# Optimization experiments

Hardware: AMD Instinct MI355X
Metric: run time of the kernel (lower is better)

## Reference

```python
import jax, jax.numpy as jnp
import numpy as np

BINS = [16]*20 + [32]*10 + [64]*5 + [65]  # sum = 1025, K = 36 bands
EMBED_DIM = 128
MAX_F = 2 * max(BINS)  # padded feature width = 130
EPS = 1e-5


def setup_inputs() -> dict:
    key = jax.random.key(0)
    ks = jax.random.split(key, 5)
    B, NB, T = 8, sum(BINS), 2048
    K = len(BINS)
    spec_ri = jax.random.normal(ks[0], (B, NB, T, 2), dtype=jnp.float32)
    # Per-band params, padded to MAX_F along the feature axis.
    gamma = jnp.ones((K, MAX_F), dtype=jnp.float32)
    beta = jnp.zeros((K, MAX_F), dtype=jnp.float32)
    W = jax.random.normal(ks[1], (K, EMBED_DIM, MAX_F), dtype=jnp.float32) * 0.05
    b = jax.random.normal(ks[2], (K, EMBED_DIM), dtype=jnp.float32) * 0.01
    return {"spec_ri": spec_ri, "gamma": gamma, "beta": beta, "W": W, "b": b}


def reference(spec_ri, gamma, beta, W, b):
    # spec_ri: (B, n_bins, T, 2) real/imag pair == torch.view_as_real(complex input)
    B, _, T, _ = spec_ri.shape
    outs = []
    start = 0
    for k, nb in enumerate(BINS):
        f = 2 * nb
        xb = spec_ri[:, start:start + nb]          # (B, nb, T, 2)
        start += nb
        # permute(0,2,1,3) then flatten -> interleaved [re0, im0, re1, im1, ...]
        x = jnp.transpose(xb, (0, 2, 1, 3)).reshape(B, T, f)  # (B, T, 2*nb)
        mu = jnp.mean(x, axis=-1, keepdims=True)
        var = jnp.mean(jnp.square(x - mu), axis=-1, keepdims=True)
        xn = (x - mu) / jnp.sqrt(var + EPS) * gamma[k, :f] + beta[k, :f]
        y = jnp.einsum('btf,ef->bte', xn, W[k, :, :f]) + b[k]  # (B, T, E)
        outs.append(jnp.transpose(y, (0, 2, 1)))   # (B, E, T)
    return jnp.stack(outs, axis=-2)                 # (B, E, K, T)
```

## Files before the change

kernel.cpp:

```cpp
#include <hip/hip_runtime.h>
#include <stdint.h>

#define T_FULL 2048
#define TT 128
#define NB_TOT 1025
#define KBANDS 36
#define EMBED 128
#define MAXF 130
#define FPAD 160
#define EPSV 1e-5f
#define LDS_W 84

typedef __attribute__((ext_vector_type(8))) short short8;
typedef __attribute__((ext_vector_type(4))) float floatx4;
typedef __attribute__((ext_vector_type(2))) float floatx2;

__device__ __forceinline__ void band_info(int band, int& nb, int& start) {
  if (band < 20)      { nb = 16; start = band << 4; }
  else if (band < 30) { nb = 32; start = 320 + ((band - 20) << 5); }
  else if (band < 35) { nb = 64; start = 640 + ((band - 30) << 6); }
  else                { nb = 65; start = 960; }
}

__device__ __forceinline__ unsigned short f2bf(float x) {
  union { float f; uint32_t u; } c; c.f = x;
  return (unsigned short)((c.u + 0x7FFFu + ((c.u >> 16) & 1u)) >> 16);
}

__global__ void __launch_bounds__(256) prep_kernel(
    const float* __restrict__ W, const float* __restrict__ gamma,
    const float* __restrict__ beta, const float* __restrict__ bvec,
    unsigned short* __restrict__ Wg, float* __restrict__ S, float* __restrict__ BB)
{
  int k = blockIdx.x;
  int w = threadIdx.x >> 6, lane = threadIdx.x & 63;
  int e = blockIdx.y * 4 + w;
  int nb, start; band_info(k, nb, start);
  int f = nb * 2;
  const float* wrow = W + ((size_t)k * EMBED + e) * MAXF;
  const float* grow = gamma + (size_t)k * MAXF;
  const float* brow = beta + (size_t)k * MAXF;
  unsigned short* orow = Wg + ((size_t)k * EMBED + e) * FPAD;

  float bb = 0.f;
  int i1 = lane, i2 = lane + 64, i3 = lane + 128;
  float v1 = 0.f, v2 = 0.f, v3 = 0.f;
  if (i1 < f) { float wv = wrow[i1]; v1 = wv * grow[i1]; bb += wv * brow[i1]; }
  if (i2 < f) { float wv = wrow[i2]; v2 = wv * grow[i2]; bb += wv * brow[i2]; }
  if (i3 < f) { float wv = wrow[i3]; v3 = wv * grow[i3]; bb += wv * brow[i3]; }
  orow[i1] = f2bf(v1);
  orow[i2] = f2bf(v2);
  if (i3 < FPAD) orow[i3] = f2bf(v3);
  float s = v1 + v2 + v3;
  #pragma unroll
  for (int off = 32; off > 0; off >>= 1) {
    s  += __shfl_down(s, off);
    bb += __shfl_down(bb, off);
  }
  if (lane == 0) {
    S[k * EMBED + e]  = s;
    BB[k * EMBED + e] = bvec[k * EMBED + e] + bb;
  }
}

__global__ void __launch_bounds__(256, 3) band_kernel(
    const float* __restrict__ spec, const unsigned short* __restrict__ Wg,
    const float* __restrict__ S, const float* __restrict__ BB,
    float* __restrict__ out)
{
  __shared__ uint32_t xn[TT * LDS_W];
  __shared__ float part_s[4][64];
  __shared__ float part_q[4][64];
  __shared__ float mu_l[TT];
  __shared__ float rs_l[TT];

  int tid = threadIdx.x;
  int w = tid >> 6, lane = tid & 63;
  int band = blockIdx.y, b = blockIdx.z;
  int t0 = blockIdx.x * TT;
  int nb, start; band_info(band, nb, start);
  int f = nb * 2;
  int ksteps = (f + 31) >> 5;

  int tl = ((w & 1) << 6) | lane;
  int swz = (tl >> 3) & 3;
  const floatx2* sp = (const floatx2*)spec +
      ((size_t)(b * NB_TOT + start) * T_FULL + (t0 + tl));
  float s = 0.f, q = 0.f;
  for (int j = (w >> 1); j < nb; j += 2) {
    floatx2 v = sp[(size_t)j * T_FULL];
    float re = v.x, im = v.y;
    s += re + im;
    q += re * re + im * im;
    xn[tl * LDS_W + (j ^ (swz << 2))] =
        (uint32_t)f2bf(re) | ((uint32_t)f2bf(im) << 16);
  }
  if (f & 31) {
    for (int idx = tid; idx < TT * 15; idx += 256) {
      int t = idx / 15, jz = 65 + idx % 15;
      xn[t * LDS_W + (jz ^ (((t >> 3) & 3) << 2))] = 0;
    }
  }
  part_s[w][lane] = s;
  part_q[w][lane] = q;
  __syncthreads();
  if (tid < TT) {
    int h = tid >> 6, li = tid & 63;
    float su = part_s[h][li] + part_s[h + 2][li];
    float sq = part_q[h][li] + part_q[h + 2][li];
    float inv_f = 1.0f / (float)f;
    float mu = su * inv_f;
    float var = sq * inv_f - mu * mu;
    mu_l[tid] = mu;
    rs_l[tid] = rsqrtf(var + EPSV);
  }
  __syncthreads();

  int lane16 = lane & 15, quad = lane >> 4;
  floatx4 acc[2][8];
  #pragma unroll
  for (int i = 0; i < 2; ++i)
    #pragma unroll
    for (int j = 0; j < 8; ++j) acc[i][j] = floatx4{0.f, 0.f, 0.f, 0.f};

  int ebase = w * 32;
  const unsigned short* wgb = Wg + ((size_t)band * EMBED + ebase) * FPAD;
  for (int kk = 0; kk < ksteps; ++kk) {
    short8 a0 = *(const short8*)(wgb + (size_t)lane16 * FPAD + kk * 32 + quad * 8);
    short8 a1 = *(const short8*)(wgb + (size_t)(16 + lane16) * FPAD + kk * 32 + quad * 8);
    #pragma unroll
    for (int nt = 0; nt < 8; ++nt) {
      int t = nt * 16 + lane16;
      int blk = kk * 4 + (quad ^ ((t >> 3) & 3));
      short8 bfr = *(const short8*)&xn[t * LDS_W + blk * 4];
      acc[0][nt] = __builtin_amdgcn_mfma_f32_16x16x32_bf16(a0, bfr, acc[0][nt], 0, 0, 0);
      acc[1][nt] = __builtin_amdgcn_mfma_f32_16x16x32_bf16(a1, bfr, acc[1][nt], 0, 0, 0);
    }
  }

  float muv[8], rsv[8];
  #pragma unroll
  for (int nt = 0; nt < 8; ++nt) {
    int t = nt * 16 + lane16;
    muv[nt] = mu_l[t];
    rsv[nt] = rs_l[t];
  }
  int obase = ((b * EMBED) * KBANDS + band) * T_FULL + t0;
  const float* Sb = S + band * EMBED + ebase;
  const float* Bb = BB + band * EMBED + ebase;
  #pragma unroll
  for (int et = 0; et < 2; ++et) {
    int e0 = et * 16 + quad * 4;
    floatx4 Sv = *(const floatx4*)(Sb + e0);
    floatx4 Bv = *(const floatx4*)(Bb + e0);
    #pragma unroll
    for (int nt = 0; nt < 8; ++nt) {
      int t = nt * 16 + lane16;
      #pragma unroll
      for (int r = 0; r < 4; ++r) {
        float y = rsv[nt] * (acc[et][nt][r] - muv[nt] * Sv[r]) + Bv[r];
        out[(size_t)obase + (size_t)(ebase + e0 + r) * (KBANDS * T_FULL) + t] = y;
      }
    }
  }
}

extern "C" void kernel_launch(void* const* d_in, const int* in_sizes, int n_in,
                              void* d_out, int out_size, void* d_ws, size_t ws_size,
                              hipStream_t stream) {
  const float* spec  = (const float*)d_in[0];
  const float* gamma = (const float*)d_in[1];
  const float* beta  = (const float*)d_in[2];
  const float* W     = (const float*)d_in[3];
  const float* bvec  = (const float*)d_in[4];
  float* out = (float*)d_out;

  unsigned short* Wg = (unsigned short*)d_ws;
  size_t wg_bytes = (size_t)KBANDS * EMBED * FPAD * sizeof(unsigned short);
  float* S  = (float*)((char*)d_ws + wg_bytes);
  float* BB = S + KBANDS * EMBED;

  prep_kernel<<<dim3(KBANDS, 32), dim3(256), 0, stream>>>(W, gamma, beta, bvec, Wg, S, BB);
  band_kernel<<<dim3(T_FULL / TT, KBANDS, 8), dim3(256), 0, stream>>>(spec, Wg, S, BB, out);
}
```

Before: 462.9 us.

## Load spectrum directly into MFMA fragments and prepack weights in fragment order

The band kernel no longer stages bf16 activations in LDS. Each wave loads its own 32 time steps straight from global memory into MFMA B-fragments and computes the per-timestep mean and variance with cross-lane shuffles, which removes both __syncthreads barriers. The prolog now writes W*gamma in a per-lane fragment layout so each A fragment is one coalesced 16-byte load. The band kernel is templated on the bin count so the K loop and its bounds checks are resolved at compile time. In exchange, every wave re-reads all 128 embedding rows of A from global memory or cache, and the per-lane global loads are 8-byte strided by T across bins.

```diff
diff --git a/kernel.cpp b/kernel.cpp
--- a/kernel.cpp
+++ b/kernel.cpp
@@ -2,18 +2,18 @@
 #include <stdint.h>
 
 #define T_FULL 2048
-#define TT 128
 #define NB_TOT 1025
 #define KBANDS 36
 #define EMBED 128
 #define MAXF 130
-#define FPAD 160
+#define KSMAX 5
 #define EPSV 1e-5f
-#define LDS_W 84
+#define ESTRIDE (KBANDS * T_FULL)
 
 typedef __attribute__((ext_vector_type(8))) short short8;
 typedef __attribute__((ext_vector_type(4))) float floatx4;
 typedef __attribute__((ext_vector_type(2))) float floatx2;
+typedef __attribute__((ext_vector_type(4))) uint32_t uint32x4;
 
 __device__ __forceinline__ void band_info(int band, int& nb, int& start) {
   if (band < 20)      { nb = 16; start = band << 4; }
@@ -27,142 +27,143 @@
   return (unsigned short)((c.u + 0x7FFFu + ((c.u >> 16) & 1u)) >> 16);
 }
 
-__global__ void __launch_bounds__(256) prep_kernel(
+__global__ void __launch_bounds__(512) prolog_kernel(
     const float* __restrict__ W, const float* __restrict__ gamma,
     const float* __restrict__ beta, const float* __restrict__ bvec,
-    unsigned short* __restrict__ Wg, float* __restrict__ S, float* __restrict__ BB)
+    unsigned short* __restrict__ A, float* __restrict__ S, float* __restrict__ BB)
 {
-  int k = blockIdx.x;
+  int band = blockIdx.x;
+  int nb, start; band_info(band, nb, start);
+  int f = nb * 2;
   int w = threadIdx.x >> 6, lane = threadIdx.x & 63;
-  int e = blockIdx.y * 4 + w;
-  int nb, start; band_info(k, nb, start);
-  int f = nb * 2;
-  const float* wrow = W + ((size_t)k * EMBED + e) * MAXF;
-  const float* grow = gamma + (size_t)k * MAXF;
-  const float* brow = beta + (size_t)k * MAXF;
-  unsigned short* orow = Wg + ((size_t)k * EMBED + e) * FPAD;
 
-  float bb = 0.f;
-  int i1 = lane, i2 = lane + 64, i3 = lane + 128;
-  float v1 = 0.f, v2 = 0.f, v3 = 0.f;
-  if (i1 < f) { float wv = wrow[i1]; v1 = wv * grow[i1]; bb += wv * brow[i1]; }
-  if (i2 < f) { float wv = wrow[i2]; v2 = wv * grow[i2]; bb += wv * brow[i2]; }
-  if (i3 < f) { float wv = wrow[i3]; v3 = wv * grow[i3]; bb += wv * brow[i3]; }
-  orow[i1] = f2bf(v1);
-  orow[i2] = f2bf(v2);
-  if (i3 < FPAD) orow[i3] = f2bf(v3);
-  float s = v1 + v2 + v3;
+  if (blockIdx.y < 16) {
+    int e = blockIdx.y * 8 + w;
+    const float* wrow = W + ((size_t)band * EMBED + e) * MAXF;
+    const float* grow = gamma + (size_t)band * MAXF;
+    const float* brow = beta + (size_t)band * MAXF;
+    float s = 0.f, bb = 0.f;
+    for (int i = lane; i < f; i += 64) {
+      float wv = wrow[i];
+      s  += wv * grow[i];
+      bb += wv * brow[i];
+    }
+    #pragma unroll
+    for (int off = 32; off > 0; off >>= 1) {
+      s  += __shfl_down(s, off);
+      bb += __shfl_down(bb, off);
+    }
+    if (lane == 0) {
+      S[band * EMBED + e]  = s;
+      BB[band * EMBED + e] = bvec[band * EMBED + e] + bb;
+    }
+  } else {
+    int kk = blockIdx.y - 16;
+    int ksteps = (f + 31) >> 5;
+    if (kk >= ksteps) return;
+    int ef = w;
+    int e = ef * 16 + (lane & 15);
+    int k0 = kk * 32 + (lane >> 4) * 8;
+    const float* wrow = W + ((size_t)band * EMBED + e) * MAXF;
+    const float* grow = gamma + (size_t)band * MAXF;
+    uint32_t u[4];
+    #pragma unroll
+    for (int p = 0; p < 4; ++p) {
+      int ka = k0 + 2 * p, kb = ka + 1;
+      float va = (ka < f) ? wrow[ka] * grow[ka] : 0.f;
+      float vb = (kb < f) ? wrow[kb] * grow[kb] : 0.f;
+      u[p] = (uint32_t)f2bf(va) | ((uint32_t)f2bf(vb) << 16);
+    }
+    uint32x4 frag = {u[0], u[1], u[2], u[3]};
+    *((uint32x4*)A + (((size_t)band * KSMAX + kk) * 8 + ef) * 64 + lane) = frag;
+  }
+}
+
+template<int NB, int KS>
+__device__ __forceinline__ void band_impl(
+    const float* __restrict__ spec, const unsigned short* __restrict__ A,
+    const float* __restrict__ S, const float* __restrict__ BB,
+    float* __restrict__ out, int band, int start)
+{
+  int tid = threadIdx.x;
+  int w = tid >> 6, lane = tid & 63;
+  int lane16 = lane & 15, quad = lane >> 4;
+  int b = blockIdx.z;
+  int t0 = blockIdx.x * 128 + w * 32;
+
+  floatx4 acc[8][2];
   #pragma unroll
-  for (int off = 32; off > 0; off >>= 1) {
-    s  += __shfl_down(s, off);
-    bb += __shfl_down(bb, off);
+  for (int ef = 0; ef < 8; ++ef) {
+    acc[ef][0] = floatx4{0.f, 0.f, 0.f, 0.f};
+    acc[ef][1] = floatx4{0.f, 0.f, 0.f, 0.f};
   }
-  if (lane == 0) {
-    S[k * EMBED + e]  = s;
-    BB[k * EMBED + e] = bvec[k * EMBED + e] + bb;
+
+  const floatx2* sp = (const floatx2*)spec +
+      ((size_t)(b * NB_TOT + start) * T_FULL + t0 + lane16);
+  const short8* ap = (const short8*)A + ((size_t)band * KSMAX * 8) * 64 + lane;
+
+  float s0 = 0.f, q0 = 0.f, s1 = 0.f, q1 = 0.f;
+  #pragma unroll 2
+  for (int kk = 0; kk < KS; ++kk) {
+    union { short8 s8; uint32_t u[4]; } b0, b1;
+    #pragma unroll
+    for (int i = 0; i < 4; ++i) {
+      int bin = kk * 16 + quad * 4 + i;
+      floatx2 v0 = floatx2{0.f, 0.f}, v1 = floatx2{0.f, 0.f};
+      if ((NB & 15) == 0 || bin < NB) {
+        v0 = sp[(size_t)bin * T_FULL];
+        v1 = sp[(size_t)bin * T_FULL + 16];
+      }
+      s0 += v0.x + v0.y; q0 += v0.x * v0.x + v0.y * v0.y;
+      s1 += v1.x + v1.y; q1 += v1.x * v1.x + v1.y * v1.y;
+      b0.u[i] = (uint32_t)f2bf(v0.x) | ((uint32_t)f2bf(v0.y) << 16);
+      b1.u[i] = (uint32_t)f2bf(v1.x) | ((uint32_t)f2bf(v1.y) << 16);
+    }
+    #pragma unroll
+    for (int ef = 0; ef < 8; ++ef) {
+      short8 a = ap[(kk * 8 + ef) * 64];
+      acc[ef][0] = __builtin_amdgcn_mfma_f32_16x16x32_bf16(a, b0.s8, acc[ef][0], 0, 0, 0);
+      acc[ef][1] = __builtin_amdgcn_mfma_f32_16x16x32_bf16(a, b1.s8, acc[ef][1], 0, 0, 0);
+    }
+  }
+
+  s0 += __shfl_xor(s0, 16); q0 += __shfl_xor(q0, 16);
+  s1 += __shfl_xor(s1, 16); q1 += __shfl_xor(q1, 16);
+  s0 += __shfl_xor(s0, 32); q0 += __shfl_xor(q0, 32);
+  s1 += __shfl_xor(s1, 32); q1 += __shfl_xor(q1, 32);
+
+  constexpr float inv_f = 1.0f / (float)(2 * NB);
+  float mu0 = s0 * inv_f, mu1 = s1 * inv_f;
+  float rs0 = rsqrtf(q0 * inv_f - mu0 * mu0 + EPSV);
+  float rs1 = rsqrtf(q1 * inv_f - mu1 * mu1 + EPSV);
+
+  size_t obase = ((size_t)(b * EMBED) * KBANDS + band) * T_FULL + t0 + lane16;
+  const float* Sb = S + band * EMBED + quad * 4;
+  const float* Bb = BB + band * EMBED + quad * 4;
+  #pragma unroll
+  for (int ef = 0; ef < 8; ++ef) {
+    floatx4 Sv = *(const floatx4*)(Sb + ef * 16);
+    floatx4 Bv = *(const floatx4*)(Bb + ef * 16);
+    size_t eb = obase + (size_t)(ef * 16 + quad * 4) * ESTRIDE;
+    #pragma unroll
+    for (int r = 0; r < 4; ++r) {
+      out[eb + (size_t)r * ESTRIDE]      = rs0 * (acc[ef][0][r] - mu0 * Sv[r]) + Bv[r];
+      out[eb + (size_t)r * ESTRIDE + 16] = rs1 * (acc[ef][1][r] - mu1 * Sv[r]) + Bv[r];
+    }
   }
 }
 
 __global__ void __launch_bounds__(256, 3) band_kernel(
-    const float* __restrict__ spec, const unsigned short* __restrict__ Wg,
+    const float* __restrict__ spec, const unsigned short* __restrict__ A,
     const float* __restrict__ S, const float* __restrict__ BB,
     float* __restrict__ out)
 {
-  __shared__ uint32_t xn[TT * LDS_W];
-  __shared__ float part_s[4][64];
-  __shared__ float part_q[4][64];
-  __shared__ float mu_l[TT];
-  __shared__ float rs_l[TT];
-
-  int tid = threadIdx.x;
-  int w = tid >> 6, lane = tid & 63;
-  int band = blockIdx.y, b = blockIdx.z;
-  int t0 = blockIdx.x * TT;
-  int nb, start; band_info(band, nb, start);
-  int f = nb * 2;
-  int ksteps = (f + 31) >> 5;
-
-  int tl = ((w & 1) << 6) | lane;
-  int swz = (tl >> 3) & 3;
-  const floatx2* sp = (const floatx2*)spec +
-      ((size_t)(b * NB_TOT + start) * T_FULL + (t0 + tl));
-  float s = 0.f, q = 0.f;
-  for (int j = (w >> 1); j < nb; j += 2) {
-    floatx2 v = sp[(size_t)j * T_FULL];
-    float re = v.x, im = v.y;
-    s += re + im;
-    q += re * re + im * im;
-    xn[tl * LDS_W + (j ^ (swz << 2))] =
-        (uint32_t)f2bf(re) | ((uint32_t)f2bf(im) << 16);
-  }
-  if (f & 31) {
-    for (int idx = tid; idx < TT * 15; idx += 256) {
-      int t = idx / 15, jz = 65 + idx % 15;
-      xn[t * LDS_W + (jz ^ (((t >> 3) & 3) << 2))] = 0;
-    }
-  }
-  part_s[w][lane] = s;
-  part_q[w][lane] = q;
-  __syncthreads();
-  if (tid < TT) {
-    int h = tid >> 6, li = tid & 63;
-    float su = part_s[h][li] + part_s[h + 2][li];
-    float sq = part_q[h][li] + part_q[h + 2][li];
-    float inv_f = 1.0f / (float)f;
-    float mu = su * inv_f;
-    float var = sq * inv_f - mu * mu;
-    mu_l[tid] = mu;
-    rs_l[tid] = rsqrtf(var + EPSV);
-  }
-  __syncthreads();
-
-  int lane16 = lane & 15, quad = lane >> 4;
-  floatx4 acc[2][8];
-  #pragma unroll
-  for (int i = 0; i < 2; ++i)
-    #pragma unroll
-    for (int j = 0; j < 8; ++j) acc[i][j] = floatx4{0.f, 0.f, 0.f, 0.f};
-
-  int ebase = w * 32;
-  const unsigned short* wgb = Wg + ((size_t)band * EMBED + ebase) * FPAD;
-  for (int kk = 0; kk < ksteps; ++kk) {
-    short8 a0 = *(const short8*)(wgb + (size_t)lane16 * FPAD + kk * 32 + quad * 8);
-    short8 a1 = *(const short8*)(wgb + (size_t)(16 + lane16) * FPAD + kk * 32 + quad * 8);
-    #pragma unroll
-    for (int nt = 0; nt < 8; ++nt) {
-      int t = nt * 16 + lane16;
-      int blk = kk * 4 + (quad ^ ((t >> 3) & 3));
-      short8 bfr = *(const short8*)&xn[t * LDS_W + blk * 4];
-      acc[0][nt] = __builtin_amdgcn_mfma_f32_16x16x32_bf16(a0, bfr, acc[0][nt], 0, 0, 0);
-      acc[1][nt] = __builtin_amdgcn_mfma_f32_16x16x32_bf16(a1, bfr, acc[1][nt], 0, 0, 0);
-    }
-  }
-
-  float muv[8], rsv[8];
-  #pragma unroll
-  for (int nt = 0; nt < 8; ++nt) {
-    int t = nt * 16 + lane16;
-    muv[nt] = mu_l[t];
-    rsv[nt] = rs_l[t];
-  }
-  int obase = ((b * EMBED) * KBANDS + band) * T_FULL + t0;
-  const float* Sb = S + band * EMBED + ebase;
-  const float* Bb = BB + band * EMBED + ebase;
-  #pragma unroll
-  for (int et = 0; et < 2; ++et) {
-    int e0 = et * 16 + quad * 4;
-    floatx4 Sv = *(const floatx4*)(Sb + e0);
-    floatx4 Bv = *(const floatx4*)(Bb + e0);
-    #pragma unroll
-    for (int nt = 0; nt < 8; ++nt) {
-      int t = nt * 16 + lane16;
-      #pragma unroll
-      for (int r = 0; r < 4; ++r) {
-        float y = rsv[nt] * (acc[et][nt][r] - muv[nt] * Sv[r]) + Bv[r];
-        out[(size_t)obase + (size_t)(ebase + e0 + r) * (KBANDS * T_FULL) + t] = y;
-      }
-    }
-  }
+  int band = blockIdx.y;
+  int nb_unused, start; band_info(band, nb_unused, start);
+  if (band < 20)      band_impl<16, 1>(spec, A, S, BB, out, band, start);
+  else if (band < 30) band_impl<32, 2>(spec, A, S, BB, out, band, start);
+  else if (band < 35) band_impl<64, 4>(spec, A, S, BB, out, band, start);
+  else                band_impl<65, 5>(spec, A, S, BB, out, band, start);
 }
 
 extern "C" void kernel_launch(void* const* d_in, const int* in_sizes, int n_in,
@@ -175,11 +176,11 @@
   const float* bvec  = (const float*)d_in[4];
   float* out = (float*)d_out;
 
-  unsigned short* Wg = (unsigned short*)d_ws;
-  size_t wg_bytes = (size_t)KBANDS * EMBED * FPAD * sizeof(unsigned short);
-  float* S  = (float*)((char*)d_ws + wg_bytes);
+  unsigned short* A = (unsigned short*)d_ws;
+  size_t a_bytes = (size_t)KBANDS * KSMAX * 8 * 64 * 16;
+  float* S  = (float*)((char*)d_ws + a_bytes);
   float* BB = S + KBANDS * EMBED;
 
-  prep_kernel<<<dim3(KBANDS, 32), dim3(256), 0, stream>>>(W, gamma, beta, bvec, Wg, S, BB);
-  band_kernel<<<dim3(T_FULL / TT, KBANDS, 8), dim3(256), 0, stream>>>(spec, Wg, S, BB, out);
+  prolog_kernel<<<dim3(KBANDS, 21), dim3(512), 0, stream>>>(W, gamma, beta, bvec, A, S, BB);
+  band_kernel<<<dim3(T_FULL / 128, KBANDS, 8), dim3(256), 0, stream>>>(spec, A, S, BB, out);
 }
```

New measurement: 414.9 us. 10.4% less time.
